# Kernel optimization log

Measured on AMD Instinct MI355X. Metric: run time of the kernel, lower is better.

Reference implementation:

```python
import jax, jax.numpy as jnp
import numpy as np

N_IN = 512    # samples per input window
N_VP = 12     # number of weighted Hermite basis functions
BATCH = 65536


def ada_weighted_hermite(n_in, n_vp, params):
    """Adaptive weighted Hermite system (VPNet-style).

    params = [dilation, translation].
    Returns phi [n_in, n_vp], dphi [n_in, 2*n_vp] (d/d dilation cols then
    d/d translation cols), ind [2, 2*n_vp] (row 0: basis index, row 1: param index).
    """
    dilation, translation = params[0], params[1]
    t = jnp.arange(n_in, dtype=params.dtype) - (n_in - 1) / 2.0  # centered grid
    xs = dilation * (t - translation)  # [n_in]
    pi14 = jnp.pi ** -0.25
    phi0 = pi14 * jnp.exp(-0.5 * xs * xs)
    phis = [phi0]
    if n_vp > 1:
        phis.append(jnp.sqrt(2.0) * xs * phi0)
    for k in range(2, n_vp):
        phis.append(jnp.sqrt(2.0 / k) * xs * phis[k - 1]
                    - jnp.sqrt((k - 1) / k) * phis[k - 2])
    phi = jnp.stack(phis, axis=1)  # [n_in, n_vp]
    # d phi_k / d xs = sqrt(2k) phi_{k-1} - xs * phi_k
    dphis = [-xs * phis[0]]
    for k in range(1, n_vp):
        dphis.append(jnp.sqrt(2.0 * k) * phis[k - 1] - xs * phis[k])
    dphi_dx = jnp.stack(dphis, axis=1)  # [n_in, n_vp]
    d_dil = dphi_dx * (t - translation)[:, None]   # chain rule: dxs/d dilation
    d_tr = -dilation * dphi_dx                     # dxs/d translation
    dphi = jnp.concatenate([d_dil, d_tr], axis=1)  # [n_in, 2*n_vp]
    ind = jnp.stack([jnp.tile(jnp.arange(n_vp), 2),
                     jnp.repeat(jnp.arange(2), n_vp)])  # [2, 2*n_vp]
    return phi, dphi, ind


def setup_inputs() -> dict:
    key = jax.random.key(0)
    kx, _ = jax.random.split(key)
    x = jax.random.normal(kx, (BATCH, N_IN), dtype=jnp.float32)
    w = jnp.array([0.1, 0.0], dtype=jnp.float32)  # [dilation, translation]
    return {"x": x, "w": w}


def reference(x, w):
    phi, dphi, ind = ada_weighted_hermite(N_IN, N_VP, w)
    phip = jnp.linalg.pinv(phi, rcond=1e-15)      # [n_vp, n_in]
    coeffs = phip @ x.T                           # [n_vp, batch]
    return coeffs.T                               # [batch, n_vp]
```

## Files before the change

### kernel.cpp

```cpp
#include <hip/hip_runtime.h>

#define N_IN 512
#define N_VP 12
#define BATCH 65536

#define WAVES 4
#define ROWS 64
#define CPW (N_IN / WAVES)
#define CHUNK 32
#define NCHW (CPW / CHUNK)

__global__ __launch_bounds__(512) void build_W_kernel(const float* __restrict__ w,
                                                      float* __restrict__ Wg) {
    __shared__ float sphiT[N_VP][N_IN];
    __shared__ float Gp[2][N_VP][N_VP];
    __shared__ float G[N_VP][N_VP], Y[N_VP][N_VP], T[N_VP][N_VP];

    const int tid = threadIdx.x;
    const float dil = w[0];
    const float tr  = w[1];

    float ph[N_VP];
    {
        const float t  = (float)tid - 0.5f * (float)(N_IN - 1);
        const float xs = dil * (t - tr);
        ph[0] = 0.7511255444649425f * expf(-0.5f * xs * xs);
        ph[1] = 1.4142135623730951f * xs * ph[0];
#pragma unroll
        for (int k = 2; k < N_VP; ++k)
            ph[k] = sqrtf(2.0f / (float)k) * xs * ph[k - 1]
                  - sqrtf((float)(k - 1) / (float)k) * ph[k - 2];
#pragma unroll
        for (int k = 0; k < N_VP; ++k) sphiT[k][tid] = ph[k];
    }
    __syncthreads();

    if (tid < 288) {
        const int p = tid >> 1;
        const int i = p / N_VP, j = p % N_VP;
        const int m0 = (tid & 1) * 256;
        const float4* __restrict__ pi = reinterpret_cast<const float4*>(&sphiT[i][m0]);
        const float4* __restrict__ pj = reinterpret_cast<const float4*>(&sphiT[j][m0]);
        float s = 0.0f;
#pragma unroll 4
        for (int q = 0; q < 64; ++q) {
            const float4 a = pi[q], b = pj[q];
            s += a.x * b.x + a.y * b.y + a.z * b.z + a.w * b.w;
        }
        Gp[tid & 1][i][j] = s;
    }
    __syncthreads();
    const int ii = (tid < 144) ? tid / N_VP : 0;
    const int jj = (tid < 144) ? tid % N_VP : 0;
    if (tid < 144) {
        G[ii][jj] = Gp[0][ii][jj] + Gp[1][ii][jj];
        Y[ii][jj] = (ii == jj) ? dil : 0.0f;
    }
    __syncthreads();

    for (int it = 0; it < 3; ++it) {
        if (tid < 144) {
            float s = 0.0f;
#pragma unroll
            for (int k = 0; k < N_VP; ++k) s += G[ii][k] * Y[k][jj];
            T[ii][jj] = s;
        }
        __syncthreads();
        float v = 0.0f;
        if (tid < 144) {
            float s = 0.0f;
#pragma unroll
            for (int k = 0; k < N_VP; ++k) s += Y[ii][k] * T[k][jj];
            v = 2.0f * Y[ii][jj] - s;
        }
        __syncthreads();
        if (tid < 144) Y[ii][jj] = v;
        __syncthreads();
    }

#pragma unroll
    for (int k = 0; k < N_VP; ++k) {
        float s = 0.0f;
#pragma unroll
        for (int j2 = 0; j2 < N_VP; ++j2) s += Y[k][j2] * ph[j2];
        Wg[tid * N_VP + k] = s;
    }
}

__global__ __launch_bounds__(256, 4) void coeffs_kernel(const float* __restrict__ x,
                                                        const float* __restrict__ Wg,
                                                        float* __restrict__ out) {
    __shared__ float sb[WAVES][ROWS][CHUNK];
    const int tid  = threadIdx.x;
    const int lane = tid & 63;
    const int s    = __builtin_amdgcn_readfirstlane(tid >> 6);
    const size_t rowbase = (size_t)blockIdx.x * ROWS;
    const float* __restrict__ xq = x + rowbase * N_IN + s * CPW;
    const float* __restrict__ wbase = Wg + s * CPW * N_VP;

    const int t0 = lane >> 3, q0 = lane & 7;
    const int gbase = t0 * N_IN + q0 * 4;
    float* const wr0 = &sb[s][0][0] + t0 * CHUNK + ((q0 ^ (t0 & 7)) << 2);

    const float* rd[8];
#pragma unroll
    for (int g = 0; g < 8; ++g)
        rd[g] = &sb[s][lane][(g ^ (lane & 7)) << 2];

#define LOADC(c, pre)                                                          \
    {                                                                          \
        _Pragma("unroll")                                                      \
        for (int i_ = 0; i_ < 8; ++i_)                                         \
            pre[i_] = *reinterpret_cast<const float4*>(                        \
                xq + gbase + i_ * 8 * N_IN + (c) * CHUNK);                     \
    }
#define STOREC(pre)                                                            \
    {                                                                          \
        _Pragma("unroll")                                                      \
        for (int i_ = 0; i_ < 8; ++i_)                                         \
            *reinterpret_cast<float4*>(wr0 + i_ * 8 * CHUNK) = pre[i_];        \
    }

    float4 preA[8], preB[8];
    LOADC(0, preA)
    STOREC(preA)
    LOADC(1, preB)

    float acc[N_VP];
#pragma unroll
    for (int k = 0; k < N_VP; ++k) acc[k] = 0.0f;

#pragma unroll
    for (int c = 0; c < NCHW; ++c) {
        const float* __restrict__ wc = wbase + c * (CHUNK * N_VP);
#pragma unroll
        for (int g = 0; g < 8; ++g) {
            const float4 xv = *reinterpret_cast<const float4*>(rd[g]);
            const float* __restrict__ w4 = wc + g * (4 * N_VP);
#pragma unroll
            for (int k = 0; k < N_VP; ++k) acc[k] = fmaf(xv.x, w4[k], acc[k]);
#pragma unroll
            for (int k = 0; k < N_VP; ++k) acc[k] = fmaf(xv.y, w4[N_VP + k], acc[k]);
#pragma unroll
            for (int k = 0; k < N_VP; ++k) acc[k] = fmaf(xv.z, w4[2 * N_VP + k], acc[k]);
#pragma unroll
            for (int k = 0; k < N_VP; ++k) acc[k] = fmaf(xv.w, w4[3 * N_VP + k], acc[k]);
        }
        if (c + 1 < NCHW) {
            if (c & 1) { STOREC(preA) } else { STOREC(preB) }
        }
        if (c + 2 < NCHW) {
            if (c & 1) { LOADC(c + 2, preB) } else { LOADC(c + 2, preA) }
        }
    }

    __syncthreads();
    float4* part4 = reinterpret_cast<float4*>(&sb[0][0][0]);
    part4[s * 192 + lane * 3 + 0] = make_float4(acc[0], acc[1], acc[2],  acc[3]);
    part4[s * 192 + lane * 3 + 1] = make_float4(acc[4], acc[5], acc[6],  acc[7]);
    part4[s * 192 + lane * 3 + 2] = make_float4(acc[8], acc[9], acc[10], acc[11]);
    __syncthreads();
    if (tid < 192) {
        const float4 v0 = part4[tid], v1 = part4[192 + tid];
        const float4 v2 = part4[384 + tid], v3 = part4[576 + tid];
        float4 r;
        r.x = (v0.x + v1.x) + (v2.x + v3.x);
        r.y = (v0.y + v1.y) + (v2.y + v3.y);
        r.z = (v0.z + v1.z) + (v2.z + v3.z);
        r.w = (v0.w + v1.w) + (v2.w + v3.w);
        reinterpret_cast<float4*>(out + rowbase * N_VP)[tid] = r;
    }
}

extern "C" void kernel_launch(void* const* d_in, const int* in_sizes, int n_in,
                              void* d_out, int out_size, void* d_ws, size_t ws_size,
                              hipStream_t stream) {
    const float* x  = (const float*)d_in[0];
    const float* w  = (const float*)d_in[1];
    float* out      = (float*)d_out;
    float* Wg       = (float*)d_ws;

    build_W_kernel<<<1, 512, 0, stream>>>(w, Wg);
    coeffs_kernel<<<BATCH / ROWS, 256, 0, stream>>>(x, Wg, out);
}
```

Baseline: 43.45 us.

## Load x in block-wide 128-column strips with coalesced rows

```diff
diff --git a/kernel.cpp b/kernel.cpp
--- a/kernel.cpp
+++ b/kernel.cpp
@@ -4,11 +4,10 @@
 #define N_VP 12
 #define BATCH 65536
 
-#define WAVES 4
 #define ROWS 64
-#define CPW (N_IN / WAVES)
-#define CHUNK 32
-#define NCHW (CPW / CHUNK)
+#define NSTRIP 4
+#define SCOLS 128
+#define SF4 (ROWS * SCOLS / 4)
 
 __global__ __launch_bounds__(512) void build_W_kernel(const float* __restrict__ w,
                                                       float* __restrict__ Wg) {
@@ -87,56 +86,48 @@
     }
 }
 
-__global__ __launch_bounds__(256, 4) void coeffs_kernel(const float* __restrict__ x,
-                                                        const float* __restrict__ Wg,
-                                                        float* __restrict__ out) {
-    __shared__ float sb[WAVES][ROWS][CHUNK];
+__global__ __launch_bounds__(256) void coeffs_kernel(const float* __restrict__ x,
+                                                     const float* __restrict__ Wg,
+                                                     float* __restrict__ out) {
+    __shared__ float4 sb[SF4];
     const int tid  = threadIdx.x;
     const int lane = tid & 63;
-    const int s    = __builtin_amdgcn_readfirstlane(tid >> 6);
+    const int g    = __builtin_amdgcn_readfirstlane(tid >> 6);
     const size_t rowbase = (size_t)blockIdx.x * ROWS;
-    const float* __restrict__ xq = x + rowbase * N_IN + s * CPW;
-    const float* __restrict__ wbase = Wg + s * CPW * N_VP;
+    const float* __restrict__ xbase = x + rowbase * N_IN;
 
-    const int t0 = lane >> 3, q0 = lane & 7;
-    const int gbase = t0 * N_IN + q0 * 4;
-    float* const wr0 = &sb[s][0][0] + t0 * CHUNK + ((q0 ^ (t0 & 7)) << 2);
+    const int r_st = tid >> 5;
+    const int cg   = tid & 31;
 
-    const float* rd[8];
-#pragma unroll
-    for (int g = 0; g < 8; ++g)
-        rd[g] = &sb[s][lane][(g ^ (lane & 7)) << 2];
+    float4 pre[8];
+#define LOADS(s)                                                               \
+    { _Pragma("unroll")                                                        \
+      for (int i_ = 0; i_ < 8; ++i_)                                           \
+        pre[i_] = *reinterpret_cast<const float4*>(                            \
+            xbase + (size_t)(i_ * 8 + r_st) * N_IN + (s) * SCOLS + cg * 4); }
+#define STORES()                                                               \
+    { _Pragma("unroll")                                                        \
+      for (int i_ = 0; i_ < 8; ++i_) {                                         \
+        const int r_ = i_ * 8 + r_st;                                          \
+        sb[r_ * 32 + (cg ^ (r_ & 7))] = pre[i_]; } }
 
-#define LOADC(c, pre)                                                          \
-    {                                                                          \
-        _Pragma("unroll")                                                      \
-        for (int i_ = 0; i_ < 8; ++i_)                                         \
-            pre[i_] = *reinterpret_cast<const float4*>(                        \
-                xq + gbase + i_ * 8 * N_IN + (c) * CHUNK);                     \
-    }
-#define STOREC(pre)                                                            \
-    {                                                                          \
-        _Pragma("unroll")                                                      \
-        for (int i_ = 0; i_ < 8; ++i_)                                         \
-            *reinterpret_cast<float4*>(wr0 + i_ * 8 * CHUNK) = pre[i_];        \
-    }
-
-    float4 preA[8], preB[8];
-    LOADC(0, preA)
-    STOREC(preA)
-    LOADC(1, preB)
+    LOADS(0)
+    STORES()
+    LOADS(1)
 
     float acc[N_VP];
 #pragma unroll
     for (int k = 0; k < N_VP; ++k) acc[k] = 0.0f;
 
+    __syncthreads();
+
 #pragma unroll
-    for (int c = 0; c < NCHW; ++c) {
-        const float* __restrict__ wc = wbase + c * (CHUNK * N_VP);
+    for (int s = 0; s < NSTRIP; ++s) {
+        const float* __restrict__ wb = Wg + (s * SCOLS + g * 32) * N_VP;
 #pragma unroll
-        for (int g = 0; g < 8; ++g) {
-            const float4 xv = *reinterpret_cast<const float4*>(rd[g]);
-            const float* __restrict__ w4 = wc + g * (4 * N_VP);
+        for (int j = 0; j < 8; ++j) {
+            const float4 xv = sb[lane * 32 + ((g * 8 + j) ^ (lane & 7))];
+            const float* __restrict__ w4 = wb + j * (4 * N_VP);
 #pragma unroll
             for (int k = 0; k < N_VP; ++k) acc[k] = fmaf(xv.x, w4[k], acc[k]);
 #pragma unroll
@@ -146,22 +137,22 @@
 #pragma unroll
             for (int k = 0; k < N_VP; ++k) acc[k] = fmaf(xv.w, w4[3 * N_VP + k], acc[k]);
         }
-        if (c + 1 < NCHW) {
-            if (c & 1) { STOREC(preA) } else { STOREC(preB) }
-        }
-        if (c + 2 < NCHW) {
-            if (c & 1) { LOADC(c + 2, preB) } else { LOADC(c + 2, preA) }
+        if (s < NSTRIP - 1) {
+            __syncthreads();
+            STORES()
+            if (s < NSTRIP - 2) LOADS(s + 2)
+            __syncthreads();
         }
     }
 
     __syncthreads();
-    float4* part4 = reinterpret_cast<float4*>(&sb[0][0][0]);
-    part4[s * 192 + lane * 3 + 0] = make_float4(acc[0], acc[1], acc[2],  acc[3]);
-    part4[s * 192 + lane * 3 + 1] = make_float4(acc[4], acc[5], acc[6],  acc[7]);
-    part4[s * 192 + lane * 3 + 2] = make_float4(acc[8], acc[9], acc[10], acc[11]);
+    float4* part4 = sb;
+    part4[g * 192 + lane * 3 + 0] = make_float4(acc[0], acc[1], acc[2],  acc[3]);
+    part4[g * 192 + lane * 3 + 1] = make_float4(acc[4], acc[5], acc[6],  acc[7]);
+    part4[g * 192 + lane * 3 + 2] = make_float4(acc[8], acc[9], acc[10], acc[11]);
     __syncthreads();
     if (tid < 192) {
-        const float4 v0 = part4[tid], v1 = part4[192 + tid];
+        const float4 v0 = part4[tid],       v1 = part4[192 + tid];
         const float4 v2 = part4[384 + tid], v3 = part4[576 + tid];
         float4 r;
         r.x = (v0.x + v1.x) + (v2.x + v3.x);
```

Result: slower. 68.68 us (+58.1%).
